# Performance work log

Hardware: AMD Instinct MI355X
Metric: run time of the kernel (lower is better)

Reference implementation:

```python
import jax, jax.numpy as jnp
import numpy as np

K = 48          # kernel_size = img_shape[axial_dim]
G = 8           # num_heads
DK = 8
DV = 16
CIN = 64
EPS = 1e-5


def _bn(x, g, b, axes):
    # training-mode batch norm (biased variance), affine
    m = jnp.mean(x, axis=axes, keepdims=True)
    v = jnp.var(x, axis=axes, keepdims=True)
    shp = [1] * x.ndim
    shp[1] = x.shape[1]
    return (x - m) * jax.lax.rsqrt(v + EPS) * g.reshape(shp) + b.reshape(shp)


def setup_inputs() -> dict:
    key = jax.random.key(0)
    ks = jax.random.split(key, 8)
    x = jax.random.normal(ks[0], (1, CIN, K, K, K), dtype=jnp.float32)
    W_kv = jax.random.normal(ks[1], (G * (DK + DV), CIN), dtype=jnp.float32) * 0.05
    W_q = jax.random.normal(ks[2], (G * DK, CIN), dtype=jnp.float32) * 0.05
    relative = jax.random.normal(ks[3], (DV + 2 * DK, 2 * K - 1), dtype=jnp.float32)
    g_kv = jnp.ones((G * (DK + DV),), jnp.float32); b_kv = jnp.zeros((G * (DK + DV),), jnp.float32)
    g_q = jnp.ones((G * DK,), jnp.float32);         b_q = jnp.zeros((G * DK,), jnp.float32)
    g_sim = jnp.ones((G * 3,), jnp.float32);        b_sim = jnp.zeros((G * 3,), jnp.float32)
    g_out = jnp.ones((G * DV * 2,), jnp.float32);   b_out = jnp.zeros((G * DV * 2,), jnp.float32)
    # flatten_index[i*K+j] = i - j + K - 1  (key index minus query index)
    flatten_index = (jnp.arange(K)[:, None] - jnp.arange(K)[None, :] + K - 1).reshape(-1).astype(jnp.int32)
    f_qr = jnp.asarray(0.1, jnp.float32); f_kr = jnp.asarray(0.1, jnp.float32)
    f_sve = jnp.asarray(0.1, jnp.float32); f_sv = jnp.asarray(1.0, jnp.float32)
    return dict(x=x, W_kv=W_kv, W_q=W_q, g_kv=g_kv, b_kv=b_kv, g_q=g_q, b_q=b_q,
                g_sim=g_sim, b_sim=b_sim, g_out=g_out, b_out=b_out,
                relative=relative, f_qr=f_qr, f_kr=f_kr, f_sv=f_sv, f_sve=f_sve,
                flatten_index=flatten_index)


def reference(x, W_kv, W_q, g_kv, b_kv, g_q, b_q, g_sim, b_sim, g_out, b_out,
              relative, f_qr, f_kr, f_sv, f_sve, flatten_index):
    N, C, H, W, D = x.shape  # axial_dim=0 -> attend over H
    B = N * W * D
    xp = jnp.transpose(x, (0, 3, 4, 1, 2)).reshape(B, C, H)  # [B, C, H]

    kv = _bn(jnp.einsum('oc,bch->boh', W_kv, xp), g_kv, b_kv, (0, 2))
    kv = kv.reshape(B, G, DK + DV, H)
    k, v = kv[:, :, :DK], kv[:, :, DK:]                       # [B,G,dk,H], [B,G,dv,H]
    q = _bn(jnp.einsum('oc,bch->boh', W_q, xp), g_q, b_q, (0, 2)).reshape(B, G, DK, H)

    emb = relative[:, flatten_index].reshape(DV + 2 * DK, K, K)
    q_emb, k_emb, v_emb = emb[:DK], emb[DK:2 * DK], emb[2 * DK:]

    qr = jnp.einsum('bgci,cij->bgij', q, q_emb) * f_qr
    kr = jnp.swapaxes(jnp.einsum('bgci,cij->bgij', k, k_emb), 2, 3) * f_kr
    qk = jnp.einsum('bgci,bgcj->bgij', q, k)

    stacked = jnp.concatenate([qk, qr, kr], axis=1)           # [B, 3G, H, H]
    stacked = _bn(stacked, g_sim, b_sim, (0, 2, 3)).reshape(B, 3, G, H, H).sum(axis=1)
    sim = jax.nn.softmax(stacked, axis=3)                     # softmax over keys j

    sv = jnp.einsum('bgij,bgcj->bgci', sim, v) * f_sv         # [B,G,dv,H]
    sve = jnp.einsum('bgij,cij->bgci', sim, v_emb) * f_sve    # [B,G,dv,H]

    out = jnp.concatenate([sv, sve], axis=-1).reshape(B, G * DV * 2, H)
    out = _bn(out, g_out, b_out, (0, 2)).reshape(N, W, D, G * DV, 2, H).sum(axis=-2)
    return jnp.transpose(out, (0, 3, 4, 1, 2))                # [N, out_planes, H, W, D]
```

## Files before the change

kernel.cpp:

```cpp
#include <hip/hip_runtime.h>


typedef unsigned short u16;
typedef __attribute__((ext_vector_type(8))) short short8v;
typedef __attribute__((ext_vector_type(4))) float float4v;

#define N_S 110592
#define N_B 2304

__device__ __forceinline__ float b2f(u16 v) {
    return __builtin_bit_cast(float, ((unsigned)v) << 16);
}
__device__ __forceinline__ u16 f2b(float f) {
    unsigned u = __builtin_bit_cast(unsigned, f);
    u = (u + 0x7FFFu + ((u >> 16) & 1u)) >> 16;
    return (u16)u;
}
__device__ __forceinline__ float ldf(const void* p, int idx, int f32) {
    return f32 ? ((const float*)p)[idx] : b2f(((const u16*)p)[idx]);
}

__global__ void k_detect(const u16* X, int* flag) {
    __shared__ int tot;
    if (threadIdx.x == 0) tot = 0;
    __syncthreads();
    int cnt = 0;
#pragma unroll
    for (int k = 0; k < 8; k++) {
        u16 v = X[(threadIdx.x * 8 + k) * 2];
        int e = (v >> 7) & 0xFF;
        cnt += (e >= 0x70 && e <= 0x8F) ? 1 : 0;
    }
    atomicAdd(&tot, cnt);
    __syncthreads();
    if (threadIdx.x == 0) flag[0] = (tot < 1024) ? 1 : 0;
}

#define ZERO_N 180800
__global__ void k_zero(float* w) {
    for (int i = blockIdx.x * blockDim.x + threadIdx.x; i < ZERO_N; i += gridDim.x * blockDim.x)
        w[i] = 0.0f;
}

__global__ void k_emb(const void* rel, const int* fidx, const int* flag,
                      u16* qe, u16* keT, u16* ve, u16* rq2, u16* rk2, u16* rv2) {
    int f32 = flag[0];
    if (blockIdx.x == 0 && threadIdx.x < 96) {
        int d = threadIdx.x;
#pragma unroll
        for (int c = 0; c < 8; c++) {
            rq2[d * 8 + c] = (d < 95) ? f2b(ldf(rel, c * 95 + d, f32)) : (u16)0;
            rk2[d * 8 + c] = (d < 95) ? f2b(ldf(rel, (8 + c) * 95 + d, f32)) : (u16)0;
        }
#pragma unroll
        for (int c = 0; c < 16; c++)
            rv2[c * 96 + d] = (d < 95) ? f2b(ldf(rel, (16 + c) * 95 + d, f32)) : (u16)0;
    }
    int t = blockIdx.x * 256 + threadIdx.x;
    if (t >= 2304) return;
    int i = t / 48, j = t % 48;
    int fij = fidx[i * 48 + j];
    int fji = fidx[j * 48 + i];
#pragma unroll
    for (int c = 0; c < 8; c++) {
        qe[c * 2304 + t]  = f2b(ldf(rel, c * 95 + fij, f32));
        keT[c * 2304 + t] = f2b(ldf(rel, (8 + c) * 95 + fji, f32));
    }
#pragma unroll
    for (int c = 0; c < 16; c++)
        ve[c * 2304 + t] = f2b(ldf(rel, (16 + c) * 95 + fij, f32));
}

__global__ void k_mtab(const void* rel, const int* flag,
                       float* mq, float* mk, float* e1q, float* e1k) {
    __shared__ float rl[1520];
    int f32 = flag[0];
    int tid = threadIdx.x;
    for (int idx = tid; idx < 1520; idx += 128) rl[idx] = ldf(rel, idx, f32);
    __syncthreads();
    if (tid >= 96) return;
    int tbl = tid / 48, i = tid % 48;
    const float* R = rl + tbl * 760;
    float* M = (tbl ? mk : mq) + i * 40;
    float* E = (tbl ? e1k : e1q) + i * 8;
    float acc[36], e[8];
#pragma unroll
    for (int x = 0; x < 36; x++) acc[x] = 0.0f;
#pragma unroll
    for (int c = 0; c < 8; c++) e[c] = 0.0f;
    for (int d = i; d < i + 48; d++) {
        float v[8];
#pragma unroll
        for (int c = 0; c < 8; c++) { v[c] = R[c * 95 + d]; e[c] += v[c]; }
        int idx = 0;
#pragma unroll
        for (int c = 0; c < 8; c++)
#pragma unroll
            for (int c2 = c; c2 < 8; c2++) { acc[idx] += v[c] * v[c2]; idx++; }
    }
    int idx = 0;
#pragma unroll
    for (int c = 0; c < 8; c++) {
        E[c] = e[c];
#pragma unroll
        for (int c2 = c; c2 < 8; c2++) {
            M[idx] = (c2 == c ? 1.0f : 2.0f) * acc[idx];
            idx++;
        }
    }
}

__global__ __launch_bounds__(256) void k_gram(const void* Xv, const int* flag,
                                              float* musumR, float* gramR) {
    __shared__ float xs[64 * 65];
    int f32 = flag[0];
    int tid = threadIdx.x;
    int rep = blockIdx.x & 7;
    int cb1 = tid >> 4, cb2 = tid & 15;
    float acc[4][4];
#pragma unroll
    for (int a = 0; a < 4; a++)
#pragma unroll
        for (int b = 0; b < 4; b++) acc[a][b] = 0.0f;
    float mur = 0.0f;
    for (int tile = blockIdx.x; tile < 1728; tile += gridDim.x) {
        int s0 = tile * 64;
        __syncthreads();
#pragma unroll
        for (int r = 0; r < 4; r++) {
            int idx4 = tid + 256 * r;
            int c = idx4 >> 4, sl = (idx4 & 15) * 4;
            if (f32) {
                float4 u = *(const float4*)((const float*)Xv + c * N_S + s0 + sl);
                xs[c * 65 + sl + 0] = u.x; xs[c * 65 + sl + 1] = u.y;
                xs[c * 65 + sl + 2] = u.z; xs[c * 65 + sl + 3] = u.w;
            } else {
                ushort4 u = *(const ushort4*)((const u16*)Xv + c * N_S + s0 + sl);
                xs[c * 65 + sl + 0] = b2f(u.x); xs[c * 65 + sl + 1] = b2f(u.y);
                xs[c * 65 + sl + 2] = b2f(u.z); xs[c * 65 + sl + 3] = b2f(u.w);
            }
        }
        __syncthreads();
        for (int s = 0; s < 64; s++) {
            float av[4], bv[4];
#pragma unroll
            for (int a = 0; a < 4; a++) av[a] = xs[(cb1 + 16 * a) * 65 + s];
#pragma unroll
            for (int b = 0; b < 4; b++) bv[b] = xs[(cb2 + 16 * b) * 65 + s];
#pragma unroll
            for (int a = 0; a < 4; a++)
#pragma unroll
                for (int b = 0; b < 4; b++) acc[a][b] += av[a] * bv[b];
        }
        if (tid < 64) {
            for (int s = 0; s < 64; s++) mur += xs[tid * 65 + s];
        }
    }
#pragma unroll
    for (int a = 0; a < 4; a++)
#pragma unroll
        for (int b = 0; b < 4; b++)
            atomicAdd(&gramR[rep * 4096 + (cb1 + 16 * a) * 64 + (cb2 + 16 * b)], acc[a][b]);
    if (tid < 64) atomicAdd(&musumR[rep * 64 + tid], mur);
}

__global__ void k_gsum(const float* musumR, const float* gramR, float* musum, float* gram) {
    int idx = blockIdx.x * 256 + threadIdx.x;
    if (idx < 4096) {
        float s = 0.0f;
#pragma unroll
        for (int r = 0; r < 8; r++) s += gramR[r * 4096 + idx];
        gram[idx] = s;
    } else if (idx < 4160) {
        int c = idx - 4096;
        float s = 0.0f;
#pragma unroll
        for (int r = 0; r < 8; r++) s += musumR[r * 64 + c];
        musum[c] = s;
    }
}

__global__ __launch_bounds__(256) void k_fold(const void* Wkv, const void* Wq,
        const void* gkv, const void* bkv, const void* gq, const void* bq,
        const int* flag, const float* musum, const float* gram,
        float* weff, u16* weffh, float* beff) {
    int f32 = flag[0];
    int o = threadIdx.x;
    float gam, bet;
    float w[64];
    if (o < 192) {
#pragma unroll
        for (int c = 0; c < 64; c++) w[c] = ldf(Wkv, o * 64 + c, f32);
        gam = ldf(gkv, o, f32); bet = ldf(bkv, o, f32);
    } else {
        int oq = o - 192;
#pragma unroll
        for (int c = 0; c < 64; c++) w[c] = ldf(Wq, oq * 64 + c, f32);
        gam = ldf(gq, oq, f32); bet = ldf(bq, oq, f32);
    }
    const float inv = 1.0f / (float)N_S;
    float mean = 0.0f;
#pragma unroll
    for (int c = 0; c < 64; c++) mean += w[c] * musum[c];
    mean *= inv;
    float e2 = 0.0f;
    for (int c = 0; c < 64; c++) {
        float t = 0.0f;
#pragma unroll
        for (int c2 = 0; c2 < 64; c2++) t += w[c2] * gram[c * 64 + c2];
        e2 += w[c] * t;
    }
    e2 *= inv;
    float var = e2 - mean * mean;
    if (var < 0.0f) var = 0.0f;
    float sc = gam * rsqrtf(var + 1e-5f);
#pragma unroll
    for (int c = 0; c < 64; c++) {
        float wv = sc * w[c];
        weff[o * 64 + c] = wv;
        weffh[o * 64 + c] = f2b(wv);
    }
    beff[o] = bet - sc * mean;
}

__global__ __launch_bounds__(256) void k_xpose(const void* Xv, const int* flag, u16* Xt) {
    __shared__ float tile[64][65];
    int f32 = flag[0];
    int h = blockIdx.x, b0 = blockIdx.y * 64, tid = threadIdx.x;
#pragma unroll
    for (int r = 0; r < 4; r++) {
        int idx = tid + 256 * r;
        int c = idx >> 4, bq = (idx & 15) * 4;
        if (f32) {
            float4 u = *(const float4*)((const float*)Xv + (size_t)c * N_S + h * 2304 + b0 + bq);
            tile[c][bq + 0] = u.x; tile[c][bq + 1] = u.y;
            tile[c][bq + 2] = u.z; tile[c][bq + 3] = u.w;
        } else {
            ushort4 u = *(const ushort4*)((const u16*)Xv + (size_t)c * N_S + h * 2304 + b0 + bq);
            tile[c][bq + 0] = b2f(u.x); tile[c][bq + 1] = b2f(u.y);
            tile[c][bq + 2] = b2f(u.z); tile[c][bq + 3] = b2f(u.w);
        }
    }
    __syncthreads();
#pragma unroll
    for (int r = 0; r < 4; r++) {
        int idx = tid + 256 * r;
        int bb = idx >> 4, cq = (idx & 15) * 4;
        ushort4 o4 = make_ushort4(f2b(tile[cq + 0][bb]), f2b(tile[cq + 1][bb]),
                                  f2b(tile[cq + 2][bb]), f2b(tile[cq + 3][bb]));
        *(ushort4*)(Xt + (size_t)(b0 + bb) * 3456 + h * 72 + cq) = o4;
    }
}

__global__ __launch_bounds__(256) void k_stage1m(const u16* Xt, const u16* weffh, const float* beff,
        const float* mq, const float* mk, const float* e1q, const float* e1k,
        float* sstatR, u16* qkv) {
    __shared__ __align__(16) u16 xs[3456];
    __shared__ __align__(16) u16 qkbf[6144];
    __shared__ float sbias[256];
    __shared__ float red[48];
    int b = blockIdx.x, tid = threadIdx.x;
    {
        const uint4* src = (const uint4*)(Xt + (size_t)b * 3456);
        uint4* dst = (uint4*)xs;
        for (int idx = tid; idx < 432; idx += 256) dst[idx] = src[idx];
    }
    sbias[tid] = beff[tid];
    if (tid < 48) red[tid] = 0.0f;
    __syncthreads();
    {
        int wv = tid >> 6, l = tid & 63;
        int lm = l & 15, lk8 = (l >> 4) * 8;
        short8v Bf[3][2];
#pragma unroll
        for (int ct = 0; ct < 3; ct++)
#pragma unroll
            for (int ks = 0; ks < 2; ks++)
                Bf[ct][ks] = *(const short8v*)(xs + (ct * 16 + lm) * 72 + ks * 32 + lk8);
        float4v acc[4][3];
#pragma unroll
        for (int a = 0; a < 4; a++)
#pragma unroll
            for (int c = 0; c < 3; c++)
#pragma unroll
                for (int e = 0; e < 4; e++) acc[a][c][e] = 0.0f;
#pragma unroll
        for (int rt = 0; rt < 4; rt++) {
            int orow = wv * 64 + rt * 16 + lm;
#pragma unroll
            for (int ks = 0; ks < 2; ks++) {
                short8v Af = *(const short8v*)(weffh + orow * 64 + ks * 32 + lk8);
#pragma unroll
                for (int ct = 0; ct < 3; ct++)
                    acc[rt][ct] = __builtin_amdgcn_mfma_f32_16x16x32_bf16(Af, Bf[ct][ks], acc[rt][ct], 0, 0, 0);
            }
        }
        int rbase = (l >> 4) * 4;
        u16* qdst = qkv + (size_t)b * 12288;
#pragma unroll
        for (int rt = 0; rt < 4; rt++) {
#pragma unroll
            for (int ct = 0; ct < 3; ct++) {
                int h = ct * 16 + lm;
#pragma unroll
                for (int rg = 0; rg < 4; rg++) {
                    int o = wv * 64 + rt * 16 + rbase + rg;
                    u16 vb = f2b(acc[rt][ct][rg] + sbias[o]);
                    int row, lq = -1;
                    if (o >= 192) {
                        int g = (o - 192) >> 3, c = (o - 192) & 7;
                        row = g * 32 + c;
                        lq = (g * 8 + c) * 48;
                    } else {
                        int g = o / 24, t = o % 24;
                        if (t < 8) { row = g * 32 + 8 + t; lq = 3072 + (g * 8 + t) * 48; }
                        else       { row = g * 32 + 16 + (t - 8); }
                    }
                    qdst[row * 48 + h] = vb;
                    if (lq >= 0) qkbf[lq + h] = vb;
                }
            }
        }
    }
    __syncthreads();
    {
        int g = tid >> 5, t = tid & 31;
        float gq[36], gk[36], sq[8], sk[8];
        float s1qr = 0, s1kr = 0, s2qr = 0, s2kr = 0;
#pragma unroll
        for (int x = 0; x < 36; x++) { gq[x] = 0.0f; gk[x] = 0.0f; }
#pragma unroll
        for (int c = 0; c < 8; c++) { sq[c] = 0.0f; sk[c] = 0.0f; }
#pragma unroll
        for (int pass = 0; pass < 2; pass++) {
            int i = t + pass * 32;
            if (i >= 48) break;
            float qv[8], kvv[8];
#pragma unroll
            for (int c = 0; c < 8; c++) {
                qv[c]  = b2f(qkbf[(g * 8 + c) * 48 + i]);
                kvv[c] = b2f(qkbf[3072 + (g * 8 + c) * 48 + i]);
            }
            const float* mqr = mq + i * 40;
            const float* mkr = mk + i * 40;
            const float* eqr = e1q + i * 8;
            const float* ekr = e1k + i * 8;
            int idx = 0;
#pragma unroll
            for (int c = 0; c < 8; c++) {
                sq[c] += qv[c]; sk[c] += kvv[c];
                s1qr += qv[c] * eqr[c];
                s1kr += kvv[c] * ekr[c];
#pragma unroll
                for (int c2 = c; c2 < 8; c2++) {
                    float oq = qv[c] * qv[c2], ok = kvv[c] * kvv[c2];
                    gq[idx] += oq; gk[idx] += ok;
                    s2qr += mqr[idx] * oq;
                    s2kr += mkr[idx] * ok;
                    idx++;
                }
            }
        }
#pragma unroll
        for (int off = 1; off <= 16; off <<= 1) {
#pragma unroll
            for (int x = 0; x < 36; x++) { gq[x] += __shfl_xor(gq[x], off); gk[x] += __shfl_xor(gk[x], off); }
#pragma unroll
            for (int c = 0; c < 8; c++) { sq[c] += __shfl_xor(sq[c], off); sk[c] += __shfl_xor(sk[c], off); }
            s1qr += __shfl_xor(s1qr, off); s1kr += __shfl_xor(s1kr, off);
            s2qr += __shfl_xor(s2qr, off); s2kr += __shfl_xor(s2kr, off);
        }
        if (t == 0) {
            float s1qk = 0.0f, s2qk = 0.0f;
            int idx = 0;
#pragma unroll
            for (int c = 0; c < 8; c++) {
                s1qk += sq[c] * sk[c];
#pragma unroll
                for (int c2 = c; c2 < 8; c2++) {
                    float w = (c2 == c) ? 1.0f : 2.0f;
                    s2qk += w * gq[idx] * gk[idx];
                    idx++;
                }
            }
            red[0 * 8 + g] = s1qk;  red[1 * 8 + g] = s1qr;  red[2 * 8 + g] = s1kr;
            red[3 * 8 + g] = s2qk;  red[4 * 8 + g] = s2qr;  red[5 * 8 + g] = s2kr;
        }
    }
    __syncthreads();
    if (tid < 48) atomicAdd(&sstatR[(b & 255) * 48 + tid], red[tid]);
}

__global__ __launch_bounds__(256) void k_stage1(const void* Xv, const float* weff, const float* beff,
        const float* mq, const float* mk, const float* e1q, const float* e1k,
        const int* flag, float* sstatR, u16* qkv) {
    __shared__ __align__(16) float xs[3072];
    __shared__ __align__(16) float qk[6144];
    __shared__ float red[48];
    int f32 = flag[0];
    int b = blockIdx.x, tid = threadIdx.x;
    for (int idx = tid; idx < 3072; idx += 256) {
        int c = idx / 48, h = idx % 48;
        xs[idx] = ldf(Xv, c * N_S + h * 2304 + b, f32);
    }
    __syncthreads();
    {
        int g = tid >> 5, r = tid & 31;
        int o;
        if (r < 8)       o = 192 + g * 8 + r;
        else if (r < 16) o = g * 24 + (r - 8);
        else             o = g * 24 + 8 + (r - 16);
        float wr[64];
        const float4* wrow = (const float4*)(weff + o * 64);
#pragma unroll
        for (int c4 = 0; c4 < 16; c4++) {
            float4 t4 = wrow[c4];
            wr[c4 * 4 + 0] = t4.x; wr[c4 * 4 + 1] = t4.y; wr[c4 * 4 + 2] = t4.z; wr[c4 * 4 + 3] = t4.w;
        }
        float bias = beff[o];
        u16* gdst = qkv + (b * 256 + tid) * 48;
        float* ldst = (r < 8) ? (qk + g * 768 + r * 48)
                    : (r < 16 ? (qk + g * 768 + 384 + (r - 8) * 48) : nullptr);
#pragma unroll
        for (int hb = 0; hb < 6; hb++) {
            float acc[8];
#pragma unroll
            for (int u = 0; u < 8; u++) acc[u] = bias;
#pragma unroll
            for (int c = 0; c < 64; c++) {
                float wv = wr[c];
                const float4* xp = (const float4*)(xs + c * 48 + hb * 8);
                float4 x0 = xp[0], x1 = xp[1];
                acc[0] += wv * x0.x; acc[1] += wv * x0.y; acc[2] += wv * x0.z; acc[3] += wv * x0.w;
                acc[4] += wv * x1.x; acc[5] += wv * x1.y; acc[6] += wv * x1.z; acc[7] += wv * x1.w;
            }
            ushort4 p0 = make_ushort4(f2b(acc[0]), f2b(acc[1]), f2b(acc[2]), f2b(acc[3]));
            ushort4 p1 = make_ushort4(f2b(acc[4]), f2b(acc[5]), f2b(acc[6]), f2b(acc[7]));
            *(ushort4*)(gdst + hb * 8)     = p0;
            *(ushort4*)(gdst + hb * 8 + 4) = p1;
            if (ldst) {
                *(float4*)(ldst + hb * 8)     = make_float4(acc[0], acc[1], acc[2], acc[3]);
                *(float4*)(ldst + hb * 8 + 4) = make_float4(acc[4], acc[5], acc[6], acc[7]);
            }
        }
    }
    __syncthreads();
    {
        int g = tid >> 5, t = tid & 31;
        float gq[36], gk[36], sq[8], sk[8];
        float s1qr = 0, s1kr = 0, s2qr = 0, s2kr = 0;
#pragma unroll
        for (int x = 0; x < 36; x++) { gq[x] = 0.0f; gk[x] = 0.0f; }
#pragma unroll
        for (int c = 0; c < 8; c++) { sq[c] = 0.0f; sk[c] = 0.0f; }
#pragma unroll
        for (int pass = 0; pass < 2; pass++) {
            int i = t + pass * 32;
            if (i >= 48) break;
            float qv[8], kvv[8];
#pragma unroll
            for (int c = 0; c < 8; c++) {
                qv[c]  = qk[g * 768 + c * 48 + i];
                kvv[c] = qk[g * 768 + 384 + c * 48 + i];
            }
            const float* mqr = mq + i * 40;
            const float* mkr = mk + i * 40;
            const float* eqr = e1q + i * 8;
            const float* ekr = e1k + i * 8;
            int idx = 0;
#pragma unroll
            for (int c = 0; c < 8; c++) {
                sq[c] += qv[c]; sk[c] += kvv[c];
                s1qr += qv[c] * eqr[c];
                s1kr += kvv[c] * ekr[c];
#pragma unroll
                for (int c2 = c; c2 < 8; c2++) {
                    float oq = qv[c] * qv[c2], ok = kvv[c] * kvv[c2];
                    gq[idx] += oq; gk[idx] += ok;
                    s2qr += mqr[idx] * oq;
                    s2kr += mkr[idx] * ok;
                    idx++;
                }
            }
        }
#pragma unroll
        for (int off = 1; off <= 16; off <<= 1) {
#pragma unroll
            for (int x = 0; x < 36; x++) { gq[x] += __shfl_xor(gq[x], off); gk[x] += __shfl_xor(gk[x], off); }
#pragma unroll
            for (int c = 0; c < 8; c++) { sq[c] += __shfl_xor(sq[c], off); sk[c] += __shfl_xor(sk[c], off); }
            s1qr += __shfl_xor(s1qr, off); s1kr += __shfl_xor(s1kr, off);
            s2qr += __shfl_xor(s2qr, off); s2kr += __shfl_xor(s2kr, off);
        }
        if (t == 0) {
            float s1qk = 0.0f, s2qk = 0.0f;
            int idx = 0;
#pragma unroll
            for (int c = 0; c < 8; c++) {
                s1qk += sq[c] * sk[c];
#pragma unroll
                for (int c2 = c; c2 < 8; c2++) {
                    float w = (c2 == c) ? 1.0f : 2.0f;
                    s2qk += w * gq[idx] * gk[idx];
                    idx++;
                }
            }
            red[0 * 8 + g] = s1qk;  red[1 * 8 + g] = s1qr;  red[2 * 8 + g] = s1kr;
            red[3 * 8 + g] = s2qk;  red[4 * 8 + g] = s2qr;  red[5 * 8 + g] = s2kr;
        }
    }
    __syncthreads();
    if (tid < 48) atomicAdd(&sstatR[(b & 255) * 48 + tid], red[tid]);
}

__global__ void k_simcoef(const float* sstatR, const void* gsim, const void* fqrp, const void* fkrp,
                          const int* flag, int scaled, float* scoef) {
    int ch = threadIdx.x;
    if (ch >= 24) return;
    int f32 = flag[0];
    float f = 1.0f;
    if (!scaled) {
        if (ch >= 16)     f = ldf(fkrp, 0, f32);
        else if (ch >= 8) f = ldf(fqrp, 0, f32);
    }
    float s1 = 0.0f, s2 = 0.0f;
#pragma unroll 8
    for (int r = 0; r < 256; r++) {
        s1 += sstatR[r * 48 + ch];
        s2 += sstatR[r * 48 + 24 + ch];
    }
    const float n = 2304.0f * 2304.0f;
    float mean = f * s1 / n;
    float var = f * f * s2 / n - mean * mean;
    if (var < 0.0f) var = 0.0f;
    scoef[ch] = ldf(gsim, ch, f32) * rsqrtf(var + 1e-5f);
}

__global__ __launch_bounds__(64) void k_attn3(const u16* qkv,
        const u16* rq2, const u16* rk2, const u16* rv2,
        const float* scoef, const void* fqrp, const void* fkrp,
        const void* fsvp, const void* fsvep, const int* flag,
        float* ostatR, u16* pre2) {
    __shared__ __align__(16) u16 qT[384];
    __shared__ __align__(16) u16 kT[384];
    __shared__ __align__(16) u16 R[8448];
    int f32 = flag[0];
    int b = blockIdx.x, g = blockIdx.y, tid = threadIdx.x;
    int lr = tid & 15, lk = tid >> 4;
    u16* qrB = R;
    u16* krB = R + 2304;
    u16* zb  = R;
    u16* zd  = R + 3456;
    const u16* src = qkv + (b * 256 + g * 32) * 48;
#pragma unroll
    for (int e = 0; e < 6; e++) {
        int idx = tid + 64 * e;
        int c = idx / 48, h = idx % 48;
        qT[h * 8 + c] = src[c * 48 + h];
        kT[h * 8 + c] = src[(8 + c) * 48 + h];
    }
    __syncthreads();
    short8v z8 = {0, 0, 0, 0, 0, 0, 0, 0};
    short8v aq[3], ak[3];
#pragma unroll
    for (int tm = 0; tm < 3; tm++) {
        aq[tm] = (lk == 0) ? *(const short8v*)(qT + (tm * 16 + lr) * 8) : z8;
        ak[tm] = (lk == 0) ? *(const short8v*)(kT + (tm * 16 + lr) * 8) : z8;
    }
#pragma unroll
    for (int tn = 0; tn < 6; tn++) {
        short8v bq = (lk == 0) ? *(const short8v*)(rq2 + (tn * 16 + lr) * 8) : z8;
        short8v bk = (lk == 0) ? *(const short8v*)(rk2 + (tn * 16 + lr) * 8) : z8;
#pragma unroll
        for (int tm = 0; tm < 3; tm++) {
            float4v a0 = {0, 0, 0, 0}, a1 = {0, 0, 0, 0};
            a0 = __builtin_amdgcn_mfma_f32_16x16x32_bf16(aq[tm], bq, a0, 0, 0, 0);
            a1 = __builtin_amdgcn_mfma_f32_16x16x32_bf16(ak[tm], bk, a1, 0, 0, 0);
#pragma unroll
            for (int r = 0; r < 4; r++) {
                int i = tm * 16 + lk * 4 + r;
                int dd = tn * 16 + lr - i;
                if (dd >= 0 && dd < 48) {
                    qrB[i * 48 + dd] = f2b(a0[r]);
                    krB[i * 56 + dd] = f2b(a1[r]);
                }
            }
        }
    }
    float4v qk[3][3];
#pragma unroll
    for (int tn = 0; tn < 3; tn++) {
        short8v bkf = (lk == 0) ? *(const short8v*)(kT + (tn * 16 + lr) * 8) : z8;
#pragma unroll
        for (int tm = 0; tm < 3; tm++) {
            float4v a = {0, 0, 0, 0};
            qk[tm][tn] = __builtin_amdgcn_mfma_f32_16x16x32_bf16(aq[tm], bkf, a, 0, 0, 0);
        }
    }
    __syncthreads();
    float fqr = ldf(fqrp, 0, f32), fkr = ldf(fkrp, 0, f32);
    float fsv = ldf(fsvp, 0, f32), fsve = ldf(fsvep, 0, f32);
    float c0 = scoef[g], c1f = scoef[8 + g] * fqr, c2f = scoef[16 + g] * fkr;
#pragma unroll
    for (int tm = 0; tm < 3; tm++)
#pragma unroll
        for (int r = 0; r < 4; r++) {
            int i = tm * 16 + lk * 4 + r;
            float v0[3];
#pragma unroll
            for (int tn = 0; tn < 3; tn++) {
                int j = tn * 16 + lr;
                v0[tn] = c0 * qk[tm][tn][r]
                       + c1f * b2f(qrB[i * 48 + 47 - j])
                       + c2f * b2f(krB[j * 56 + 47 - i]);
            }
            float m = fmaxf(fmaxf(v0[0], v0[1]), v0[2]);
#pragma unroll
            for (int off = 1; off <= 8; off <<= 1) m = fmaxf(m, __shfl_xor(m, off));
            float e0 = __expf(v0[0] - m), e1 = __expf(v0[1] - m), e2 = __expf(v0[2] - m);
            float s = e0 + e1 + e2;
#pragma unroll
            for (int off = 1; off <= 8; off <<= 1) s += __shfl_xor(s, off);
            float inv = 1.0f / s;
            qk[tm][0][r] = e0 * inv;
            qk[tm][1][r] = e1 * inv;
            qk[tm][2][r] = e2 * inv;
        }
    __syncthreads();
#pragma unroll
    for (int e = 0; e < 17; e++) {
        int idx = tid + 64 * e;
        if (idx < 1056) {
            uint4 zz = {0, 0, 0, 0};
            ((uint4*)R)[idx] = zz;
        }
    }
    __syncthreads();
#pragma unroll
    for (int tm = 0; tm < 3; tm++)
#pragma unroll
        for (int r = 0; r < 4; r++) {
            int i = tm * 16 + lk * 4 + r;
#pragma unroll
            for (int tn = 0; tn < 3; tn++) {
                int j = tn * 16 + lr;
                u16 pb = f2b(qk[tm][tn][r]);
                zb[i * 72 + j] = pb;
                zd[i * 104 + i + 47 - j] = pb;
            }
        }
    __syncthreads();
    float4v sv[3], se[3];
#pragma unroll
    for (int tm = 0; tm < 3; tm++) { sv[tm] = (float4v){0,0,0,0}; se[tm] = (float4v){0,0,0,0}; }
#pragma unroll
    for (int ks = 0; ks < 2; ks++) {
        short8v bv = (ks == 0 || lk < 2) ? *(const short8v*)(src + (16 + lr) * 48 + ks * 32 + lk * 8) : z8;
#pragma unroll
        for (int tm = 0; tm < 3; tm++) {
            short8v af = *(const short8v*)(zb + (tm * 16 + lr) * 72 + ks * 32 + lk * 8);
            sv[tm] = __builtin_amdgcn_mfma_f32_16x16x32_bf16(af, bv, sv[tm], 0, 0, 0);
        }
    }
#pragma unroll
    for (int ks = 0; ks < 3; ks++) {
        short8v br = *(const short8v*)(rv2 + lr * 96 + ks * 32 + lk * 8);
#pragma unroll
        for (int tm = 0; tm < 3; tm++) {
            short8v ad = *(const short8v*)(zd + (tm * 16 + lr) * 104 + ks * 32 + lk * 8);
            se[tm] = __builtin_amdgcn_mfma_f32_16x16x32_bf16(ad, br, se[tm], 0, 0, 0);
        }
    }
    int c = lr;
    float sA = 0, qA = 0, sB = 0, qB = 0;
    u16* pdst = pre2 + ((b * 128 + g * 16 + c) * 48) * 2;
#pragma unroll
    for (int tm = 0; tm < 3; tm++)
#pragma unroll
        for (int r = 0; r < 4; r++) {
            int i = tm * 16 + lk * 4 + r;
            float a = sv[tm][r] * fsv, bb = se[tm][r] * fsve;
            *(ushort2*)(pdst + i * 2) = make_ushort2(f2b(a), f2b(bb));
            sA += a; qA += a * a; sB += bb; qB += bb * bb;
        }
    sA += __shfl_xor(sA, 16); qA += __shfl_xor(qA, 16);
    sB += __shfl_xor(sB, 16); qB += __shfl_xor(qB, 16);
    sA += __shfl_xor(sA, 32); qA += __shfl_xor(qA, 32);
    sB += __shfl_xor(sB, 32); qB += __shfl_xor(qB, 32);
    if (lk == 0) {
        int ch2 = g * 32 + c * 2;
        float* od = ostatR + (b & 255) * 512;
        atomicAdd(&od[ch2 * 2 + 0], sA);
        atomicAdd(&od[ch2 * 2 + 1], qA);
        atomicAdd(&od[ch2 * 2 + 2], sB);
        atomicAdd(&od[ch2 * 2 + 3], qB);
    }
}

__global__ void k_outcoef(const float* ostatR, const void* gout, const void* bout,
                          const int* flag, float* ocoef) {
    int f32 = flag[0];
    int o = threadIdx.x;
    float s1 = 0.0f, s2 = 0.0f;
#pragma unroll 8
    for (int r = 0; r < 256; r++) {
        s1 += ostatR[r * 512 + o * 2];
        s2 += ostatR[r * 512 + o * 2 + 1];
    }
    const float n = 110592.0f;
    float mean = s1 / n;
    float var = s2 / n - mean * mean;
    if (var < 0.0f) var = 0.0f;
    float sc = ldf(gout, o, f32) * rsqrtf(var + 1e-5f);
    ocoef[o * 2] = sc;
    ocoef[o * 2 + 1] = ldf(bout, o, f32) - mean * sc;
}

__global__ __launch_bounds__(256) void k_final(const u16* pre2, const float* ocoef,
                                               const int* flag, void* outp) {
    __shared__ float tile[48 * 49];
    int f32 = flag[0];
    int ch = blockIdx.x, w = blockIdx.y, tid = threadIdx.x;
    float sc0 = ocoef[(ch * 2) * 2],     sh0 = ocoef[(ch * 2) * 2 + 1];
    float sc1 = ocoef[(ch * 2 + 1) * 2], sh1 = ocoef[(ch * 2 + 1) * 2 + 1];
    float shs = sh0 + sh1;
#pragma unroll
    for (int r = 0; r < 9; r++) {
        int idx = tid + 256 * r;
        int d = idx / 48, i = idx % 48;
        ushort2 p = ((const ushort2*)pre2)[((w * 48 + d) * 128 + ch) * 48 + i];
        tile[d * 49 + i] = b2f(p.x) * sc0 + b2f(p.y) * sc1 + shs;
    }
    __syncthreads();
#pragma unroll
    for (int r = 0; r < 9; r++) {
        int idx = tid + 256 * r;
        int i = idx / 48, d = idx % 48;
        float v = tile[d * 49 + i];
        int oidx = ch * N_S + i * 2304 + w * 48 + d;
        if (f32) ((float*)outp)[oidx] = v;
        else     ((u16*)outp)[oidx] = f2b(v);
    }
}

__global__ __launch_bounds__(256) void k_qkstat(const void* Xv, const float* weff, const float* beff,
        const u16* qe, const u16* keT, const void* fqrp, const void* fkrp,
        const int* flag, float* sstatR) {
    __shared__ __align__(16) float xs[3072];
    __shared__ __align__(16) float qsh[3072];
    __shared__ __align__(16) float ksh[3072];
    __shared__ float red[48];
    int f32 = flag[0];
    int b = blockIdx.x, tid = threadIdx.x;
    for (int idx = tid; idx < 3072; idx += 256) {
        int c = idx / 48, h = idx % 48;
        xs[idx] = ldf(Xv, c * N_S + h * 2304 + b, f32);
    }
    if (tid < 48) red[tid] = 0.0f;
    __syncthreads();
    {
        int r = tid >> 1, half = tid & 1;
        int o; float* dst;
        if (r < 64) { o = 192 + r; dst = qsh + r * 48; }
        else { int rk = r - 64; o = (rk >> 3) * 24 + (rk & 7); dst = ksh + rk * 48; }
        float wr[64];
        const float4* wrow = (const float4*)(weff + o * 64);
#pragma unroll
        for (int c4 = 0; c4 < 16; c4++) {
            float4 t4 = wrow[c4];
            wr[c4 * 4 + 0] = t4.x; wr[c4 * 4 + 1] = t4.y; wr[c4 * 4 + 2] = t4.z; wr[c4 * 4 + 3] = t4.w;
        }
        float bias = beff[o];
        int h0 = half * 24;
#pragma unroll
        for (int hb = 0; hb < 3; hb++) {
            float acc[8];
#pragma unroll
            for (int u = 0; u < 8; u++) acc[u] = bias;
#pragma unroll
            for (int c = 0; c < 64; c++) {
                float wv = wr[c];
                const float4* xp = (const float4*)(xs + c * 48 + h0 + hb * 8);
                float4 x0 = xp[0], x1 = xp[1];
                acc[0] += wv * x0.x; acc[1] += wv * x0.y; acc[2] += wv * x0.z; acc[3] += wv * x0.w;
                acc[4] += wv * x1.x; acc[5] += wv * x1.y; acc[6] += wv * x1.z; acc[7] += wv * x1.w;
            }
            *(float4*)(dst + h0 + hb * 8)     = make_float4(acc[0], acc[1], acc[2], acc[3]);
            *(float4*)(dst + h0 + hb * 8 + 4) = make_float4(acc[4], acc[5], acc[6], acc[7]);
        }
    }
    __syncthreads();
    float fqr = ldf(fqrp, 0, f32), fkr = ldf(fkrp, 0, f32);
    float sum[24], sq[24];
#pragma unroll
    for (int k = 0; k < 24; k++) { sum[k] = 0.0f; sq[k] = 0.0f; }
    for (int r = 0; r < 3; r++) {
        int chunk = tid + 256 * r;
        if (chunk >= 576) break;
        int i = chunk / 12, j0 = (chunk % 12) * 4;
        float qv[8][4], kv[8][4];
#pragma unroll
        for (int c = 0; c < 8; c++) {
            ushort4 uq = *(const ushort4*)(qe + c * 2304 + i * 48 + j0);
            ushort4 uk = *(const ushort4*)(keT + c * 2304 + i * 48 + j0);
            qv[c][0] = b2f(uq.x); qv[c][1] = b2f(uq.y); qv[c][2] = b2f(uq.z); qv[c][3] = b2f(uq.w);
            kv[c][0] = b2f(uk.x); kv[c][1] = b2f(uk.y); kv[c][2] = b2f(uk.z); kv[c][3] = b2f(uk.w);
        }
#pragma unroll
        for (int g = 0; g < 8; g++) {
            float zq[4] = {0,0,0,0}, zr[4] = {0,0,0,0}, zk[4] = {0,0,0,0};
#pragma unroll
            for (int c = 0; c < 8; c++) {
                float qi = qsh[(g * 8 + c) * 48 + i];
                float4 kk = *(const float4*)(ksh + (g * 8 + c) * 48 + j0);
                zq[0] += qi * kk.x; zq[1] += qi * kk.y; zq[2] += qi * kk.z; zq[3] += qi * kk.w;
                zr[0] += qi * qv[c][0]; zr[1] += qi * qv[c][1]; zr[2] += qi * qv[c][2]; zr[3] += qi * qv[c][3];
                zk[0] += kk.x * kv[c][0]; zk[1] += kk.y * kv[c][1]; zk[2] += kk.z * kv[c][2]; zk[3] += kk.w * kv[c][3];
            }
#pragma unroll
            for (int u = 0; u < 4; u++) {
                float a = zq[u];        sum[g] += a;       sq[g] += a * a;
                float r1 = zr[u] * fqr; sum[8 + g] += r1;  sq[8 + g] += r1 * r1;
                float r2 = zk[u] * fkr; sum[16 + g] += r2; sq[16 + g] += r2 * r2;
            }
        }
    }
#pragma unroll
    for (int k = 0; k < 24; k++) {
        float s = sum[k], q = sq[k];
        for (int off = 32; off >= 1; off >>= 1) { s += __shfl_xor(s, off); q += __shfl_xor(q, off); }
        if ((tid & 63) == 0) { atomicAdd(&red[k], s); atomicAdd(&red[24 + k], q); }
    }
    __syncthreads();
    if (tid < 48) atomicAdd(&sstatR[(b & 255) * 48 + tid], red[tid]);
}

__global__ __launch_bounds__(256) void k_attn(const void* Xv, const float* weff, const float* beff,
        const u16* qe, const u16* keT, const u16* ve,
        const float* scoef, const float* ocoef,
        const void* fqrp, const void* fkrp, const void* fsvp, const void* fsvep,
        const int* flag, float* ostatR, void* outp, int mode) {
    __shared__ __align__(16) float zx[3072];
    __shared__ __align__(16) float qsh[3072];
    __shared__ __align__(16) float ksh[3072];
    __shared__ __align__(16) float vsh[6144];
    __shared__ float osl[512];
    int f32 = flag[0];
    int b = blockIdx.x, tid = threadIdx.x;
    for (int idx = tid; idx < 3072; idx += 256) {
        int c = idx / 48, h = idx % 48;
        zx[idx] = ldf(Xv, c * N_S + h * 2304 + b, f32);
    }
    __syncthreads();
    {
        int o; float* dst;
        if (tid < 64)       { o = 192 + tid; dst = qsh + tid * 48; }
        else if (tid < 128) { int rk = tid - 64; o = (rk >> 3) * 24 + (rk & 7); dst = ksh + rk * 48; }
        else                { int rv = tid - 128; o = (rv >> 4) * 24 + 8 + (rv & 15); dst = vsh + rv * 48; }
        float wr[64];
        const float4* wrow = (const float4*)(weff + o * 64);
#pragma unroll
        for (int c4 = 0; c4 < 16; c4++) {
            float4 t4 = wrow[c4];
            wr[c4 * 4 + 0] = t4.x; wr[c4 * 4 + 1] = t4.y; wr[c4 * 4 + 2] = t4.z; wr[c4 * 4 + 3] = t4.w;
        }
        float bias = beff[o];
#pragma unroll
        for (int hb = 0; hb < 6; hb++) {
            float acc[8];
#pragma unroll
            for (int u = 0; u < 8; u++) acc[u] = bias;
#pragma unroll
            for (int c = 0; c < 64; c++) {
                float wv = wr[c];
                const float4* xp = (const float4*)(zx + c * 48 + hb * 8);
                float4 x0 = xp[0], x1 = xp[1];
                acc[0] += wv * x0.x; acc[1] += wv * x0.y; acc[2] += wv * x0.z; acc[3] += wv * x0.w;
                acc[4] += wv * x1.x; acc[5] += wv * x1.y; acc[6] += wv * x1.z; acc[7] += wv * x1.w;
            }
            *(float4*)(dst + hb * 8)     = make_float4(acc[0], acc[1], acc[2], acc[3]);
            *(float4*)(dst + hb * 8 + 4) = make_float4(acc[4], acc[5], acc[6], acc[7]);
        }
    }
    __syncthreads();
    float fqr = ldf(fqrp, 0, f32), fkr = ldf(fkrp, 0, f32);
    float fsv = ldf(fsvp, 0, f32), fsve = ldf(fsvep, 0, f32);
    float* z = zx;
    for (int g = 0; g < 8; g++) {
        float c0 = scoef[g], c1 = scoef[8 + g], c2 = scoef[16 + g];
        for (int r = 0; r < 3; r++) {
            int chunk = tid + 256 * r;
            if (chunk >= 576) break;
            int i = chunk / 12, j0 = (chunk % 12) * 4;
            float zq[4] = {0,0,0,0}, zr[4] = {0,0,0,0}, zk[4] = {0,0,0,0};
#pragma unroll
            for (int c = 0; c < 8; c++) {
                ushort4 uq = *(const ushort4*)(qe + c * 2304 + i * 48 + j0);
                ushort4 uk = *(const ushort4*)(keT + c * 2304 + i * 48 + j0);
                float qi = qsh[(g * 8 + c) * 48 + i];
                float4 kk = *(const float4*)(ksh + (g * 8 + c) * 48 + j0);
                zq[0] += qi * kk.x; zq[1] += qi * kk.y; zq[2] += qi * kk.z; zq[3] += qi * kk.w;
                zr[0] += qi * b2f(uq.x); zr[1] += qi * b2f(uq.y); zr[2] += qi * b2f(uq.z); zr[3] += qi * b2f(uq.w);
                zk[0] += kk.x * b2f(uk.x); zk[1] += kk.y * b2f(uk.y); zk[2] += kk.z * b2f(uk.z); zk[3] += kk.w * b2f(uk.w);
            }
            float4 o4;
            o4.x = c0 * zq[0] + c1 * (fqr * zr[0]) + c2 * (fkr * zk[0]);
            o4.y = c0 * zq[1] + c1 * (fqr * zr[1]) + c2 * (fkr * zk[1]);
            o4.z = c0 * zq[2] + c1 * (fqr * zr[2]) + c2 * (fkr * zk[2]);
            o4.w = c0 * zq[3] + c1 * (fqr * zr[3]) + c2 * (fkr * zk[3]);
            *(float4*)(z + i * 52 + j0) = o4;
        }
        __syncthreads();
        {
            int wv = tid >> 6, lane = tid & 63;
            for (int rr = 0; rr < 12; rr++) {
                int i = wv * 12 + rr;
                float val = (lane < 48) ? z[i * 52 + lane] : -1e30f;
                float m = val;
                for (int off = 32; off >= 1; off >>= 1) m = fmaxf(m, __shfl_xor(m, off));
                float e = (lane < 48) ? __expf(val - m) : 0.0f;
                float s = e;
                for (int off = 32; off >= 1; off >>= 1) s += __shfl_xor(s, off);
                if (lane < 48) z[i * 52 + lane] = e / s;
            }
        }
        __syncthreads();
        {
            int c = tid >> 4, u = tid & 15;
            int ch2 = g * 32 + c * 2;
            float oc0 = 0, oc1 = 0, osh = 0;
            if (mode != 0) {
                oc0 = ocoef[ch2 * 2]; oc1 = ocoef[(ch2 + 1) * 2];
                osh = ocoef[ch2 * 2 + 1] + ocoef[(ch2 + 1) * 2 + 1];
            }
            float sumA = 0, sqA = 0, sumB = 0, sqB = 0;
#pragma unroll
            for (int r = 0; r < 3; r++) {
                int i = u + 16 * r;
                float sv = 0.0f, se = 0.0f;
#pragma unroll
                for (int j4 = 0; j4 < 12; j4++) {
                    float4 sm = *(const float4*)(z + i * 52 + j4 * 4);
                    float4 vv = *(const float4*)(vsh + (g * 16 + c) * 48 + j4 * 4);
                    ushort4 veu = *(const ushort4*)(ve + c * 2304 + i * 48 + j4 * 4);
                    sv += sm.x * vv.x + sm.y * vv.y + sm.z * vv.z + sm.w * vv.w;
                    se += sm.x * b2f(veu.x) + sm.y * b2f(veu.y) + sm.z * b2f(veu.z) + sm.w * b2f(veu.w);
                }
                float a = sv * fsv, bb = se * fsve;
                if (mode == 0) {
                    sumA += a; sqA += a * a; sumB += bb; sqB += bb * bb;
                } else {
                    float outv = a * oc0 + bb * oc1 + osh;
                    int oidx = (g * 16 + c) * N_S + i * 2304 + b;
                    if (f32) ((float*)outp)[oidx] = outv;
                    else     ((u16*)outp)[oidx] = f2b(outv);
                }
            }
            if (mode == 0) {
                for (int off = 1; off <= 8; off <<= 1) {
                    sumA += __shfl_xor(sumA, off); sqA += __shfl_xor(sqA, off);
                    sumB += __shfl_xor(sumB, off); sqB += __shfl_xor(sqB, off);
                }
                if (u == 0) {
                    int base = ch2 * 2;
                    osl[base + 0] = sumA; osl[base + 1] = sqA;
                    osl[base + 2] = sumB; osl[base + 3] = sqB;
                }
            }
        }
        __syncthreads();
    }
    if (mode == 0) {
        float* od = ostatR + (b & 255) * 512;
        atomicAdd(&od[tid], osl[tid]);
        atomicAdd(&od[tid + 256], osl[tid + 256]);
    }
}

extern "C" void kernel_launch(void* const* d_in, const int* in_sizes, int n_in,
                              void* d_out, int out_size, void* d_ws, size_t ws_size,
                              hipStream_t stream) {
    const void* X    = d_in[0];
    const void* Wkv  = d_in[1];
    const void* Wq   = d_in[2];
    const void* gkv  = d_in[3];
    const void* bkv  = d_in[4];
    const void* gq   = d_in[5];
    const void* bq   = d_in[6];
    const void* gsim = d_in[7];
    const void* gout = d_in[9];
    const void* bout = d_in[10];
    const void* rel  = d_in[11];
    const void* fqrp = d_in[12];
    const void* fkrp = d_in[13];
    const void* fsvp = d_in[14];
    const void* fsvep= d_in[15];
    const int* fidx  = (const int*)d_in[16];

    float* W      = (float*)d_ws;
    float* musum  = W;
    float* gram   = W + 64;
    float* musumR = W + 4160;
    float* gramR  = W + 4672;
    float* sstatR = W + 37440;
    float* ostatR = W + 49728;
    float* weff   = W + 180800;
    float* beff   = W + 197184;
    float* scoef  = W + 197440;
    float* ocoef  = W + 197464;
    int*   flag   = (int*)(W + 197976);
    float* mq     = W + 197980;
    float* mk     = W + 199900;
    float* e1q    = W + 201820;
    float* e1k    = W + 202204;
    u16*   qe     = (u16*)(W + 202588);
    u16*   keT    = (u16*)(W + 211804);
    u16*   ve     = (u16*)(W + 221020);
    u16*   weffh  = (u16*)(W + 239452);
    u16*   rq2    = (u16*)(W + 247644);
    u16*   rk2    = (u16*)(W + 248028);
    u16*   rv2    = (u16*)(W + 248412);
    u16*   qkv    = (u16*)(W + 249180);
    u16*   pre2   = qkv + 28311552;
    u16*   Xt     = (u16*)(W + 28560732);

    const size_t need1 = (size_t)28560732 * 4;
    const size_t need2 = (size_t)32542044 * 4;
    const int tier = (ws_size >= need2) ? 2 : ((ws_size >= need1) ? 1 : 0);

    k_detect<<<1, 256, 0, stream>>>((const u16*)X, flag);
    k_zero<<<180, 256, 0, stream>>>(W);
    k_emb<<<9, 256, 0, stream>>>(rel, fidx, flag, qe, keT, ve, rq2, rk2, rv2);
    k_gram<<<256, 256, 0, stream>>>(X, flag, musumR, gramR);
    k_gsum<<<17, 256, 0, stream>>>(musumR, gramR, musum, gram);
    k_fold<<<1, 256, 0, stream>>>(Wkv, Wq, gkv, bkv, gq, bq, flag, musum, gram, weff, weffh, beff);
    if (tier > 0) {
        k_mtab<<<1, 128, 0, stream>>>(rel, flag, mq, mk, e1q, e1k);
        if (tier == 2) {
            k_xpose<<<dim3(48, 36), 256, 0, stream>>>(X, flag, Xt);
            k_stage1m<<<2304, 256, 0, stream>>>(Xt, weffh, beff, mq, mk, e1q, e1k, sstatR, qkv);
        } else {
            k_stage1<<<2304, 256, 0, stream>>>(X, weff, beff, mq, mk, e1q, e1k, flag, sstatR, qkv);
        }
        k_simcoef<<<1, 32, 0, stream>>>(sstatR, gsim, fqrp, fkrp, flag, 0, scoef);
        k_attn3<<<dim3(2304, 8), 64, 0, stream>>>(qkv, rq2, rk2, rv2, scoef,
                                                  fqrp, fkrp, fsvp, fsvep, flag, ostatR, pre2);
        k_outcoef<<<1, 256, 0, stream>>>(ostatR, gout, bout, flag, ocoef);
        k_final<<<dim3(128, 48), 256, 0, stream>>>(pre2, ocoef, flag, d_out);
    } else {
        k_qkstat<<<2304, 256, 0, stream>>>(X, weff, beff, qe, keT, fqrp, fkrp, flag, sstatR);
        k_simcoef<<<1, 32, 0, stream>>>(sstatR, gsim, fqrp, fkrp, flag, 1, scoef);
        k_attn<<<2304, 256, 0, stream>>>(X, weff, beff, qe, keT, ve, scoef, ocoef,
                                         fqrp, fkrp, fsvp, fsvep, flag, ostatR, d_out, 0);
        k_outcoef<<<1, 256, 0, stream>>>(ostatR, gout, bout, flag, ocoef);
        k_attn<<<2304, 256, 0, stream>>>(X, weff, beff, qe, keT, ve, scoef, ocoef,
                                         fqrp, fkrp, fsvp, fsvep, flag, ostatR, d_out, 2);
    }
}
```

Baseline: 562.5 us.

## Compute Gram matrix with MFMA on transposed bf16 input; stage qkv in LDS

Moves the transpose kernel earlier so the Gram/mean statistics pass can read the bf16 transposed layout and compute X·Xᵀ with bf16 MFMA instructions instead of scalar FMAs. Separately, stage1m now assembles the whole qkv tile in shared memory and writes it to global with coalesced 16-byte stores instead of scattered 2-byte stores. The Gram is now accumulated from bf16-rounded inputs, which may slightly change the BN statistics, and the new kernel uses more LDS.

After: 556.1 us. No clear change (-1.1%).

```diff
diff --git a/kernel.cpp b/kernel.cpp
--- a/kernel.cpp
+++ b/kernel.cpp
@@ -164,6 +164,55 @@
     if (tid < 64) atomicAdd(&musumR[rep * 64 + tid], mur);
 }
 
+__global__ __launch_bounds__(256) void k_gramm(const u16* Xt, float* musumR, float* gramR) {
+    __shared__ __align__(16) u16 xl[64 * 136];
+    int tid = threadIdx.x;
+    int rep = blockIdx.x & 7;
+    int wv = tid >> 6, l = tid & 63, lm = l & 15, lk = l >> 4;
+    int cc = tid & 63, part = tid >> 6;
+    float4v acc[4];
+#pragma unroll
+    for (int t = 0; t < 4; t++)
+#pragma unroll
+        for (int e = 0; e < 4; e++) acc[t][e] = 0.0f;
+    float msum = 0.0f;
+    for (int ch = blockIdx.x; ch < 864; ch += 256) {
+        __syncthreads();
+#pragma unroll
+        for (int e = 0; e < 4; e++) {
+            int idx = tid + 256 * e;
+            int r = idx >> 3, c8 = (idx & 7) * 8;
+            uint4 u = *(const uint4*)(Xt + (size_t)(ch * 128 + r) * 72 + c8);
+            const u16* up = (const u16*)&u;
+#pragma unroll
+            for (int j = 0; j < 8; j++) xl[(c8 + j) * 136 + r] = up[j];
+        }
+        __syncthreads();
+#pragma unroll
+        for (int rr = 0; rr < 32; rr++) msum += b2f(xl[cc * 136 + part * 32 + rr]);
+#pragma unroll
+        for (int ks = 0; ks < 4; ks++) {
+            short8v fr[4];
+#pragma unroll
+            for (int tc = 0; tc < 4; tc++)
+                fr[tc] = *(const short8v*)(xl + (tc * 16 + lm) * 136 + ks * 32 + lk * 8);
+            short8v fa = fr[wv];
+#pragma unroll
+            for (int tc = 0; tc < 4; tc++)
+                acc[tc] = __builtin_amdgcn_mfma_f32_16x16x32_bf16(fa, fr[tc], acc[tc], 0, 0, 0);
+        }
+    }
+#pragma unroll
+    for (int tc = 0; tc < 4; tc++)
+#pragma unroll
+        for (int rr = 0; rr < 4; rr++) {
+            int row = wv * 16 + lk * 4 + rr;
+            int col = tc * 16 + lm;
+            atomicAdd(&gramR[rep * 4096 + row * 64 + col], acc[tc][rr]);
+        }
+    atomicAdd(&musumR[rep * 64 + cc], msum);
+}
+
 __global__ void k_gsum(const float* musumR, const float* gramR, float* musum, float* gram) {
     int idx = blockIdx.x * 256 + threadIdx.x;
     if (idx < 4096) {
@@ -256,7 +305,7 @@
         const float* mq, const float* mk, const float* e1q, const float* e1k,
         float* sstatR, u16* qkv) {
     __shared__ __align__(16) u16 xs[3456];
-    __shared__ __align__(16) u16 qkbf[6144];
+    __shared__ __align__(16) u16 qall[12288];
     __shared__ float sbias[256];
     __shared__ float red[48];
     int b = blockIdx.x, tid = threadIdx.x;
@@ -296,7 +345,6 @@
             }
         }
         int rbase = (l >> 4) * 4;
-        u16* qdst = qkv + (size_t)b * 12288;
 #pragma unroll
         for (int rt = 0; rt < 4; rt++) {
 #pragma unroll
@@ -306,23 +354,27 @@
                 for (int rg = 0; rg < 4; rg++) {
                     int o = wv * 64 + rt * 16 + rbase + rg;
                     u16 vb = f2b(acc[rt][ct][rg] + sbias[o]);
-                    int row, lq = -1;
+                    int row;
                     if (o >= 192) {
                         int g = (o - 192) >> 3, c = (o - 192) & 7;
                         row = g * 32 + c;
-                        lq = (g * 8 + c) * 48;
                     } else {
                         int g = o / 24, t = o % 24;
-                        if (t < 8) { row = g * 32 + 8 + t; lq = 3072 + (g * 8 + t) * 48; }
-                        else       { row = g * 32 + 16 + (t - 8); }
+                        if (t < 8) row = g * 32 + 8 + t;
+                        else       row = g * 32 + 16 + (t - 8);
                     }
-                    qdst[row * 48 + h] = vb;
-                    if (lq >= 0) qkbf[lq + h] = vb;
+                    qall[row * 48 + h] = vb;
                 }
             }
         }
     }
     __syncthreads();
+    {
+        uint4* gq = (uint4*)(qkv + (size_t)b * 12288);
+        const uint4* lq = (const uint4*)qall;
+#pragma unroll
+        for (int e = 0; e < 6; e++) gq[tid + 256 * e] = lq[tid + 256 * e];
+    }
     {
         int g = tid >> 5, t = tid & 31;
         float gq[36], gk[36], sq[8], sk[8];
@@ -338,8 +390,8 @@
             float qv[8], kvv[8];
 #pragma unroll
             for (int c = 0; c < 8; c++) {
-                qv[c]  = b2f(qkbf[(g * 8 + c) * 48 + i]);
-                kvv[c] = b2f(qkbf[3072 + (g * 8 + c) * 48 + i]);
+                qv[c]  = b2f(qall[(g * 32 + c) * 48 + i]);
+                kvv[c] = b2f(qall[(g * 32 + 8 + c) * 48 + i]);
             }
             const float* mqr = mq + i * 40;
             const float* mkr = mk + i * 40;
@@ -1031,13 +1083,17 @@
     k_detect<<<1, 256, 0, stream>>>((const u16*)X, flag);
     k_zero<<<180, 256, 0, stream>>>(W);
     k_emb<<<9, 256, 0, stream>>>(rel, fidx, flag, qe, keT, ve, rq2, rk2, rv2);
-    k_gram<<<256, 256, 0, stream>>>(X, flag, musumR, gramR);
+    if (tier == 2) {
+        k_xpose<<<dim3(48, 36), 256, 0, stream>>>(X, flag, Xt);
+        k_gramm<<<256, 256, 0, stream>>>(Xt, musumR, gramR);
+    } else {
+        k_gram<<<256, 256, 0, stream>>>(X, flag, musumR, gramR);
+    }
     k_gsum<<<17, 256, 0, stream>>>(musumR, gramR, musum, gram);
     k_fold<<<1, 256, 0, stream>>>(Wkv, Wq, gkv, bkv, gq, bq, flag, musum, gram, weff, weffh, beff);
     if (tier > 0) {
         k_mtab<<<1, 128, 0, stream>>>(rel, flag, mq, mk, e1q, e1k);
         if (tier == 2) {
-            k_xpose<<<dim3(48, 36), 256, 0, stream>>>(X, flag, Xt);
             k_stage1m<<<2304, 256, 0, stream>>>(Xt, weffh, beff, mq, mk, e1q, e1k, sstatR, qkv);
         } else {
             k_stage1<<<2304, 256, 0, stream>>>(X, weff, beff, mq, mk, e1q, e1k, flag, sstatR, qkv);
```
